# Kernel tuning notes

Measured on AMD Instinct MI355X. Metric: run time of the kernel, lower is better.

## Reference

```python
import jax, jax.numpy as jnp
import numpy as np
import math

INPUT_DIM = 1024
HIDDEN_DIM = 1024
NUM_HEADS = 16
NUM_KEYS = 4096
BATCH = 1024
BETA = 8.0


def setup_inputs() -> dict:
    key = jax.random.key(0)
    kx, kk, kv = jax.random.split(key, 3)
    bound_k = 1.0 / math.sqrt(INPUT_DIM)
    bound_v = 1.0 / math.sqrt(HIDDEN_DIM)
    x = jax.random.normal(kx, (BATCH, INPUT_DIM), dtype=jnp.float32)
    keys = jax.random.uniform(kk, (NUM_KEYS * NUM_HEADS, INPUT_DIM), dtype=jnp.float32,
                              minval=-bound_k, maxval=bound_k)
    values = jax.random.uniform(kv, (NUM_KEYS * NUM_HEADS, HIDDEN_DIM), dtype=jnp.float32,
                                minval=-bound_v, maxval=bound_v)
    return {"x": x, "keys": keys, "values": values}


def reference(x, keys, values):
    scale = math.sqrt(INPUT_DIM)
    b = x.shape[0]
    # [B, num_keys*num_heads]
    weights = (x @ keys.T) / scale
    # view as [B, num_keys, num_heads]; softmax over num_keys per head
    weights = weights.reshape(b, NUM_KEYS, NUM_HEADS)
    probs = jax.nn.softmax(BETA * weights, axis=1)
    probs = probs.reshape(b, NUM_KEYS * NUM_HEADS)
    # value retrieval
    out = probs @ values  # [B, hidden_dim]
    return out
```

## Files before the change

### kernel.cpp

```cpp
#include <hip/hip_runtime.h>
#include <hip/hip_bf16.h>
#include <stdint.h>

#define BATCH  1024
#define DIM    1024
#define NKH    65536
#define NKEYS  4096
#define HID    1024

#define SC1 0.36067376022224085f

typedef __bf16 bf16x8 __attribute__((ext_vector_type(8)));
typedef float  f32x4  __attribute__((ext_vector_type(4)));

__device__ __forceinline__ unsigned short f2bf(float f) {
  union { float f; unsigned int u; } v; v.f = f;
  unsigned int r = v.u + 0x7fffu + ((v.u >> 16) & 1u);
  return (unsigned short)(r >> 16);
}
__device__ __forceinline__ float bf2f(unsigned short s) {
  union { unsigned int u; float f; } v; v.u = ((unsigned int)s) << 16;
  return v.f;
}
__device__ __forceinline__ unsigned int pk2(float lo, float hi) {
  union { __hip_bfloat162 h; unsigned int u; } v;
  v.h = __float22bfloat162_rn(make_float2(lo, hi));
  return v.u;
}
__device__ __forceinline__ void gl2lds16(const void* g, void* l) {
  __builtin_amdgcn_global_load_lds(
      (const __attribute__((address_space(1))) void*)g,
      (__attribute__((address_space(3))) void*)l, 16, 0, 0);
}

#define KEY_GROUPS (NKH * (DIM / 8))
__global__ __launch_bounds__(256) void k_cast_all(
    const float* __restrict__ keys, const float* __restrict__ x,
    unsigned short* __restrict__ Kb, unsigned short* __restrict__ Xb) {
  int i = blockIdx.x * 256 + threadIdx.x;
  if (i < KEY_GROUPS) {
    int row = i >> 7, seg = i & 127;
    int n2 = ((row & 15) << 12) | (row >> 4);
    float4 a = ((const float4*)keys)[(size_t)i * 2];
    float4 b = ((const float4*)keys)[(size_t)i * 2 + 1];
    uint4 o;
    o.x = pk2(a.x, a.y); o.y = pk2(a.z, a.w);
    o.z = pk2(b.x, b.y); o.w = pk2(b.z, b.w);
    ((uint4*)Kb)[((size_t)n2 << 7) | seg] = o;
  } else {
    int j = i - KEY_GROUPS;
    if (j < BATCH * (DIM / 8)) {
      float4 a = ((const float4*)x)[(size_t)j * 2];
      float4 b = ((const float4*)x)[(size_t)j * 2 + 1];
      uint4 o;
      o.x = pk2(a.x, a.y); o.y = pk2(a.z, a.w);
      o.z = pk2(b.x, b.y); o.w = pk2(b.z, b.w);
      ((uint4*)Xb)[j] = o;
    }
  }
}

__global__ __launch_bounds__(256) void k_transpose_cast(
    const float* __restrict__ V, unsigned short* __restrict__ vT) {
  __shared__ float tile[64][65];
  const int t = threadIdx.x;
  const int nk0 = blockIdx.x * 64;
  const int h   = blockIdx.x >> 6;
  const int k0  = (blockIdx.x & 63) * 64;
  const int j0  = blockIdx.y * 64;
  #pragma unroll
  for (int i = 0; i < 4; ++i) {
    int idx = t + i * 256;
    int row = idx >> 4, c4 = (idx & 15) << 2;
    float4 v = *(const float4*)(V + (size_t)((k0 + row) * 16 + h) * HID + (j0 + c4));
    tile[row][c4 + 0] = v.x; tile[row][c4 + 1] = v.y;
    tile[row][c4 + 2] = v.z; tile[row][c4 + 3] = v.w;
  }
  __syncthreads();
  const int q = t & 7, jj = t >> 3;
  #pragma unroll
  for (int i = 0; i < 2; ++i) {
    int j = jj + i * 32;
    uint4 o;
    o.x = pk2(tile[q*8+0][j], tile[q*8+1][j]);
    o.y = pk2(tile[q*8+2][j], tile[q*8+3][j]);
    o.z = pk2(tile[q*8+4][j], tile[q*8+5][j]);
    o.w = pk2(tile[q*8+6][j], tile[q*8+7][j]);
    *(uint4*)(vT + (size_t)(j0 + j) * NKH + (nk0 + q*8)) = o;
  }
}

__global__ __launch_bounds__(256) void k_gemm1_exp(
    const unsigned short* __restrict__ Xb, const unsigned short* __restrict__ Kb,
    unsigned short* __restrict__ E, float* __restrict__ denom) {
  __shared__ __align__(16) unsigned short As[128 * 32];
  __shared__ __align__(16) unsigned short Bs[128 * 32];
  __shared__ float dsum[128];
  const int t = threadIdx.x;
  const int bm = blockIdx.x & 7, bn = blockIdx.x >> 3;
  const int m0 = bm << 7, n0 = bn << 7;
  const int lane = t & 63, wave = t >> 6;
  const int wm = (wave >> 1) << 6, wn = (wave & 1) << 6;
  const int r16 = lane & 15, quad = lane >> 4;
  const int srow = lane >> 2, kseg = (lane & 3) * 8;
  const int c0 = wave * 2, c1 = wave * 2 + 1;
  const unsigned short* gA0 = Xb + (size_t)(m0 + c0*16 + srow) * DIM + kseg;
  const unsigned short* gA1 = Xb + (size_t)(m0 + c1*16 + srow) * DIM + kseg;
  const unsigned short* gB0 = Kb + (size_t)(n0 + c0*16 + srow) * DIM + kseg;
  const unsigned short* gB1 = Kb + (size_t)(n0 + c1*16 + srow) * DIM + kseg;
  if (t < 128) dsum[t] = 0.0f;
  f32x4 acc[4][4] = {};
  for (int ks = 0; ks < DIM; ks += 32) {
    __syncthreads();
    gl2lds16(gA0 + ks, As + c0 * 512);
    gl2lds16(gA1 + ks, As + c1 * 512);
    gl2lds16(gB0 + ks, Bs + c0 * 512);
    gl2lds16(gB1 + ks, Bs + c1 * 512);
    __syncthreads();
    bf16x8 af[4], bfr[4];
    #pragma unroll
    for (int mi = 0; mi < 4; ++mi)
      af[mi] = *(const bf16x8*)(As + (wm + mi*16 + r16) * 32 + quad * 8);
    #pragma unroll
    for (int ni = 0; ni < 4; ++ni)
      bfr[ni] = *(const bf16x8*)(Bs + (wn + ni*16 + r16) * 32 + quad * 8);
    #pragma unroll
    for (int mi = 0; mi < 4; ++mi)
      #pragma unroll
      for (int ni = 0; ni < 4; ++ni)
        acc[mi][ni] = __builtin_amdgcn_mfma_f32_16x16x32_bf16(af[mi], bfr[ni], acc[mi][ni], 0, 0, 0);
  }
  float rs[16] = {0,0,0,0,0,0,0,0,0,0,0,0,0,0,0,0};
  #pragma unroll
  for (int mi = 0; mi < 4; ++mi) {
    #pragma unroll
    for (int ni = 0; ni < 4; ++ni) {
      #pragma unroll
      for (int v = 0; v < 4; ++v) {
        float e = exp2f(acc[mi][ni][v] * SC1);
        int row = m0 + wm + mi*16 + quad*4 + v;
        int col = n0 + wn + ni*16 + r16;
        E[(size_t)row * NKH + col] = f2bf(e);
        rs[mi*4 + v] += e;
      }
    }
  }
  #pragma unroll
  for (int m = 1; m < 16; m <<= 1)
    #pragma unroll
    for (int i = 0; i < 16; ++i) rs[i] += __shfl_xor(rs[i], m);
  if (r16 == 0) {
    #pragma unroll
    for (int i = 0; i < 16; ++i)
      atomicAdd(&dsum[wm + (i >> 2)*16 + quad*4 + (i & 3)], rs[i]);
  }
  __syncthreads();
  const int h = n0 >> 12;
  if (t < 128) atomicAdd(&denom[(size_t)(m0 + t) * 16 + h], dsum[t]);
}

__global__ __launch_bounds__(256) void k_gemm2(
    const unsigned short* __restrict__ P, const unsigned short* __restrict__ Vt,
    float* __restrict__ out, const float* __restrict__ denom) {
  __shared__ __align__(16) unsigned short As[128 * 32];
  __shared__ __align__(16) unsigned short Bs[128 * 32];
  const int t = threadIdx.x;
  const int nwg = 1024, cpx = nwg >> 3;
  const int lb = (blockIdx.x & 7) * cpx + (blockIdx.x >> 3);
  const int bm = lb & 7, bn = (lb >> 3) & 7, sp = lb >> 6;
  const int m0 = bm << 7, n0 = bn << 7;
  const size_t kb = (size_t)sp * (NKH / 16);
  const int lane = t & 63, wave = t >> 6;
  const int wm = (wave >> 1) << 6, wn = (wave & 1) << 6;
  const int r16 = lane & 15, quad = lane >> 4;
  const int srow = lane >> 2, kseg = (lane & 3) * 8;
  const int c0 = wave * 2, c1 = wave * 2 + 1;
  const unsigned short* gA0 = P  + (size_t)(m0 + c0*16 + srow) * NKH + kb + kseg;
  const unsigned short* gA1 = P  + (size_t)(m0 + c1*16 + srow) * NKH + kb + kseg;
  const unsigned short* gB0 = Vt + (size_t)(n0 + c0*16 + srow) * NKH + kb + kseg;
  const unsigned short* gB1 = Vt + (size_t)(n0 + c1*16 + srow) * NKH + kb + kseg;
  f32x4 acc[4][4] = {};
  for (int ks = 0; ks < NKH / 16; ks += 32) {
    __syncthreads();
    gl2lds16(gA0 + ks, As + c0 * 512);
    gl2lds16(gA1 + ks, As + c1 * 512);
    gl2lds16(gB0 + ks, Bs + c0 * 512);
    gl2lds16(gB1 + ks, Bs + c1 * 512);
    __syncthreads();
    bf16x8 af[4], bfr[4];
    #pragma unroll
    for (int mi = 0; mi < 4; ++mi)
      af[mi] = *(const bf16x8*)(As + (wm + mi*16 + r16) * 32 + quad * 8);
    #pragma unroll
    for (int ni = 0; ni < 4; ++ni)
      bfr[ni] = *(const bf16x8*)(Bs + (wn + ni*16 + r16) * 32 + quad * 8);
    #pragma unroll
    for (int mi = 0; mi < 4; ++mi)
      #pragma unroll
      for (int ni = 0; ni < 4; ++ni)
        acc[mi][ni] = __builtin_amdgcn_mfma_f32_16x16x32_bf16(af[mi], bfr[ni], acc[mi][ni], 0, 0, 0);
  }
  #pragma unroll
  for (int mi = 0; mi < 4; ++mi) {
    float rr[4];
    #pragma unroll
    for (int v = 0; v < 4; ++v) {
      int row = m0 + wm + mi*16 + quad*4 + v;
      rr[v] = 1.0f / denom[(size_t)row * 16 + sp];
    }
    #pragma unroll
    for (int ni = 0; ni < 4; ++ni) {
      #pragma unroll
      for (int v = 0; v < 4; ++v) {
        int row = m0 + wm + mi*16 + quad*4 + v;
        int col = n0 + wn + ni*16 + r16;
        unsafeAtomicAdd(&out[(size_t)row * HID + col], acc[mi][ni][v] * rr[v]);
      }
    }
  }
}

extern "C" void kernel_launch(void* const* d_in, const int* in_sizes, int n_in,
                              void* d_out, int out_size, void* d_ws, size_t ws_size,
                              hipStream_t stream) {
  (void)in_sizes; (void)n_in; (void)out_size; (void)ws_size;
  const float* x      = (const float*)d_in[0];
  const float* keys   = (const float*)d_in[1];
  const float* values = (const float*)d_in[2];
  float* out = (float*)d_out;

  unsigned short* E  = (unsigned short*)d_ws;
  unsigned short* B2 = E + (size_t)BATCH * NKH;
  unsigned short* Xb = B2 + (size_t)NKH * DIM;
  float* denom = (float*)(Xb + (size_t)BATCH * DIM);

  hipMemsetAsync(d_out, 0, (size_t)BATCH * HID * sizeof(float), stream);
  hipMemsetAsync(denom, 0, (size_t)BATCH * 16 * sizeof(float), stream);
  k_cast_all<<<(KEY_GROUPS + BATCH * (DIM / 8) + 255) / 256, 256, 0, stream>>>(
      keys, x, B2, Xb);
  k_gemm1_exp<<<(BATCH / 128) * (NKH / 128), 256, 0, stream>>>(Xb, B2, E, denom);
  k_transpose_cast<<<dim3(NKH / 64, HID / 64), 256, 0, stream>>>(values, B2);
  k_gemm2<<<(BATCH / 128) * (HID / 128) * 16, 256, 0, stream>>>(E, B2, out, denom);
}
```

Measured before the change: 1.037 ms.

## Rewrite both GEMMs with 256x256 tiles, double-buffered swizzled LDS pipeline

Both bf16 GEMMs now share a core with 256x256 block tiles, 512 threads, K-step 64, XOR-swizzled LDS and double buffering. Global-to-LDS loads for the next tile are interleaved with MFMA phases using partial vmcnt waits and setprio. The two memsets are folded into the cast and transpose kernels to cut launches. The larger tiles raise data reuse and overlap loads with compute, at the cost of more registers and LDS and fewer workgroups.

```diff
diff --git a/kernel.cpp b/kernel.cpp
--- a/kernel.cpp
+++ b/kernel.cpp
@@ -18,10 +18,6 @@
   unsigned int r = v.u + 0x7fffu + ((v.u >> 16) & 1u);
   return (unsigned short)(r >> 16);
 }
-__device__ __forceinline__ float bf2f(unsigned short s) {
-  union { unsigned int u; float f; } v; v.u = ((unsigned int)s) << 16;
-  return v.f;
-}
 __device__ __forceinline__ unsigned int pk2(float lo, float hi) {
   union { __hip_bfloat162 h; unsigned int u; } v;
   v.h = __float22bfloat162_rn(make_float2(lo, hi));
@@ -34,9 +30,12 @@
 }
 
 #define KEY_GROUPS (NKH * (DIM / 8))
+#define X_GROUPS   (BATCH * (DIM / 8))
+#define DN_GROUPS  (BATCH * 16 / 4)
 __global__ __launch_bounds__(256) void k_cast_all(
     const float* __restrict__ keys, const float* __restrict__ x,
-    unsigned short* __restrict__ Kb, unsigned short* __restrict__ Xb) {
+    unsigned short* __restrict__ Kb, unsigned short* __restrict__ Xb,
+    float* __restrict__ denom) {
   int i = blockIdx.x * 256 + threadIdx.x;
   if (i < KEY_GROUPS) {
     int row = i >> 7, seg = i & 127;
@@ -47,27 +46,36 @@
     o.x = pk2(a.x, a.y); o.y = pk2(a.z, a.w);
     o.z = pk2(b.x, b.y); o.w = pk2(b.z, b.w);
     ((uint4*)Kb)[((size_t)n2 << 7) | seg] = o;
+  } else if (i < KEY_GROUPS + X_GROUPS) {
+    int j = i - KEY_GROUPS;
+    float4 a = ((const float4*)x)[(size_t)j * 2];
+    float4 b = ((const float4*)x)[(size_t)j * 2 + 1];
+    uint4 o;
+    o.x = pk2(a.x, a.y); o.y = pk2(a.z, a.w);
+    o.z = pk2(b.x, b.y); o.w = pk2(b.z, b.w);
+    ((uint4*)Xb)[j] = o;
   } else {
-    int j = i - KEY_GROUPS;
-    if (j < BATCH * (DIM / 8)) {
-      float4 a = ((const float4*)x)[(size_t)j * 2];
-      float4 b = ((const float4*)x)[(size_t)j * 2 + 1];
-      uint4 o;
-      o.x = pk2(a.x, a.y); o.y = pk2(a.z, a.w);
-      o.z = pk2(b.x, b.y); o.w = pk2(b.z, b.w);
-      ((uint4*)Xb)[j] = o;
-    }
-  }
-}
-
-__global__ __launch_bounds__(256) void k_transpose_cast(
-    const float* __restrict__ V, unsigned short* __restrict__ vT) {
+    int d = i - KEY_GROUPS - X_GROUPS;
+    if (d < DN_GROUPS) ((float4*)denom)[d] = make_float4(0.f, 0.f, 0.f, 0.f);
+  }
+}
+
+__global__ __launch_bounds__(256) void k_fuse_vt(
+    const float* __restrict__ V, unsigned short* __restrict__ vT,
+    float* __restrict__ out) {
+  const int bid = blockIdx.x;
+  const int t = threadIdx.x;
+  if (bid >= 16384) {
+    int zi = (bid - 16384) * 256 + t;
+    ((float4*)out)[zi] = make_float4(0.f, 0.f, 0.f, 0.f);
+    return;
+  }
   __shared__ float tile[64][65];
-  const int t = threadIdx.x;
-  const int nk0 = blockIdx.x * 64;
-  const int h   = blockIdx.x >> 6;
-  const int k0  = (blockIdx.x & 63) * 64;
-  const int j0  = blockIdx.y * 64;
+  const int bx = bid & 1023, by = bid >> 10;
+  const int nk0 = bx * 64;
+  const int h   = bx >> 6;
+  const int k0  = (bx & 63) * 64;
+  const int j0  = by * 64;
   #pragma unroll
   for (int i = 0; i < 4; ++i) {
     int idx = t + i * 256;
@@ -90,130 +98,204 @@
   }
 }
 
-__global__ __launch_bounds__(256) void k_gemm1_exp(
+#define PH_WAIT4 do { asm volatile("s_waitcnt vmcnt(4)" ::: "memory"); \
+                      __builtin_amdgcn_s_barrier();                    \
+                      asm volatile("" ::: "memory"); } while (0)
+#define PH_BAR   do { __builtin_amdgcn_s_barrier();                    \
+                      asm volatile("" ::: "memory"); } while (0)
+
+__device__ __forceinline__ void gemm_core(
+    const unsigned short* __restrict__ A, const unsigned short* __restrict__ B,
+    size_t lda, size_t ldb, int m0, int n0, size_t k0, int nt,
+    unsigned short* As, unsigned short* Bs, f32x4 (&acc)[8][4]) {
+  const int t = threadIdx.x, lane = t & 63, w = t >> 6;
+  const int wr = w >> 2, wc = w & 3;
+  const int r16 = lane & 15, quad = lane >> 4;
+  const int srow = (w << 3) + (lane >> 3);
+  const int ksl  = (((lane & 7) ^ (lane >> 3)) << 3);
+  const int e8   = r16 & 7;
+  const int sq0  = ((quad ^ e8) << 3);
+  const int sq1  = (((4 + quad) ^ e8) << 3);
+  const unsigned short* Ag[2][2];
+  const unsigned short* Bg[2][2];
+  const int bsw = srow + (srow & 32);
+  #pragma unroll
+  for (int h = 0; h < 2; ++h)
+    #pragma unroll
+    for (int l = 0; l < 2; ++l) {
+      Ag[h][l] = A + (size_t)(m0 + h*64 + l*128 + srow) * lda + k0 + ksl;
+      Bg[h][l] = B + (size_t)(n0 + h*32 + l*128 + bsw)  * ldb + k0 + ksl;
+    }
+  const int wrow = w << 3;
+  const int boff = wrow + ((w >= 4) ? 32 : 0);
+  const int dAr[2][2] = {{ (wrow)*64,      (128 + wrow)*64 },
+                         { (64 + wrow)*64, (192 + wrow)*64 }};
+  const int dBr[2][2] = {{ (boff)*64,      (128 + boff)*64 },
+                         { (32 + boff)*64, (160 + boff)*64 }};
+  gl2lds16(Ag[0][0], As + dAr[0][0]); gl2lds16(Ag[0][1], As + dAr[0][1]);
+  gl2lds16(Bg[0][0], Bs + dBr[0][0]); gl2lds16(Bg[0][1], Bs + dBr[0][1]);
+  gl2lds16(Bg[1][0], Bs + dBr[1][0]); gl2lds16(Bg[1][1], Bs + dBr[1][1]);
+  gl2lds16(Ag[1][0], As + dAr[1][0]); gl2lds16(Ag[1][1], As + dAr[1][1]);
+
+  bf16x8 am[4][2], bn_[4][2];
+  for (int tt = 0; tt < nt; ++tt) {
+    unsigned short* Asc = As + ((tt & 1) << 14);
+    unsigned short* Bsc = Bs + ((tt & 1) << 14);
+    unsigned short* Asn = As + ((~tt & 1) << 14);
+    unsigned short* Bsn = Bs + ((~tt & 1) << 14);
+    const size_t kn = (size_t)((tt + 1 < nt) ? (tt + 1) : tt) * 64;
+    PH_WAIT4;
+    gl2lds16(Ag[0][0] + kn, Asn + dAr[0][0]);
+    gl2lds16(Ag[0][1] + kn, Asn + dAr[0][1]);
+    #pragma unroll
+    for (int mi = 0; mi < 4; ++mi) {
+      const unsigned short* p = Asc + (wr*128 + mi*16 + r16) * 64;
+      am[mi][0] = *(const bf16x8*)(p + sq0);
+      am[mi][1] = *(const bf16x8*)(p + sq1);
+    }
+    #pragma unroll
+    for (int ni = 0; ni < 2; ++ni) {
+      const unsigned short* p = Bsc + (wc*64 + ni*16 + r16) * 64;
+      bn_[ni][0] = *(const bf16x8*)(p + sq0);
+      bn_[ni][1] = *(const bf16x8*)(p + sq1);
+    }
+    __builtin_amdgcn_s_setprio(1);
+    #pragma unroll
+    for (int mi = 0; mi < 4; ++mi)
+      #pragma unroll
+      for (int ni = 0; ni < 2; ++ni) {
+        acc[mi][ni] = __builtin_amdgcn_mfma_f32_16x16x32_bf16(am[mi][0], bn_[ni][0], acc[mi][ni], 0, 0, 0);
+        acc[mi][ni] = __builtin_amdgcn_mfma_f32_16x16x32_bf16(am[mi][1], bn_[ni][1], acc[mi][ni], 0, 0, 0);
+      }
+    __builtin_amdgcn_s_setprio(0);
+    PH_WAIT4;
+    gl2lds16(Bg[0][0] + kn, Bsn + dBr[0][0]);
+    gl2lds16(Bg[0][1] + kn, Bsn + dBr[0][1]);
+    #pragma unroll
+    for (int ni = 2; ni < 4; ++ni) {
+      const unsigned short* p = Bsc + (wc*64 + ni*16 + r16) * 64;
+      bn_[ni][0] = *(const bf16x8*)(p + sq0);
+      bn_[ni][1] = *(const bf16x8*)(p + sq1);
+    }
+    __builtin_amdgcn_s_setprio(1);
+    #pragma unroll
+    for (int mi = 0; mi < 4; ++mi)
+      #pragma unroll
+      for (int ni = 2; ni < 4; ++ni) {
+        acc[mi][ni] = __builtin_amdgcn_mfma_f32_16x16x32_bf16(am[mi][0], bn_[ni][0], acc[mi][ni], 0, 0, 0);
+        acc[mi][ni] = __builtin_amdgcn_mfma_f32_16x16x32_bf16(am[mi][1], bn_[ni][1], acc[mi][ni], 0, 0, 0);
+      }
+    __builtin_amdgcn_s_setprio(0);
+    PH_WAIT4;
+    gl2lds16(Bg[1][0] + kn, Bsn + dBr[1][0]);
+    gl2lds16(Bg[1][1] + kn, Bsn + dBr[1][1]);
+    #pragma unroll
+    for (int mi = 0; mi < 4; ++mi) {
+      const unsigned short* p = Asc + (wr*128 + 64 + mi*16 + r16) * 64;
+      am[mi][0] = *(const bf16x8*)(p + sq0);
+      am[mi][1] = *(const bf16x8*)(p + sq1);
+    }
+    __builtin_amdgcn_s_setprio(1);
+    #pragma unroll
+    for (int mi = 0; mi < 4; ++mi)
+      #pragma unroll
+      for (int ni = 0; ni < 2; ++ni) {
+        acc[mi+4][ni] = __builtin_amdgcn_mfma_f32_16x16x32_bf16(am[mi][0], bn_[ni][0], acc[mi+4][ni], 0, 0, 0);
+        acc[mi+4][ni] = __builtin_amdgcn_mfma_f32_16x16x32_bf16(am[mi][1], bn_[ni][1], acc[mi+4][ni], 0, 0, 0);
+      }
+    __builtin_amdgcn_s_setprio(0);
+    PH_BAR;
+    gl2lds16(Ag[1][0] + kn, Asn + dAr[1][0]);
+    gl2lds16(Ag[1][1] + kn, Asn + dAr[1][1]);
+    __builtin_amdgcn_s_setprio(1);
+    #pragma unroll
+    for (int mi = 0; mi < 4; ++mi)
+      #pragma unroll
+      for (int ni = 2; ni < 4; ++ni) {
+        acc[mi+4][ni] = __builtin_amdgcn_mfma_f32_16x16x32_bf16(am[mi][0], bn_[ni][0], acc[mi+4][ni], 0, 0, 0);
+        acc[mi+4][ni] = __builtin_amdgcn_mfma_f32_16x16x32_bf16(am[mi][1], bn_[ni][1], acc[mi+4][ni], 0, 0, 0);
+      }
+    __builtin_amdgcn_s_setprio(0);
+  }
+}
+
+__global__ __launch_bounds__(512, 2) void k_gemm1_exp(
     const unsigned short* __restrict__ Xb, const unsigned short* __restrict__ Kb,
     unsigned short* __restrict__ E, float* __restrict__ denom) {
-  __shared__ __align__(16) unsigned short As[128 * 32];
-  __shared__ __align__(16) unsigned short Bs[128 * 32];
-  __shared__ float dsum[128];
+  __shared__ __align__(16) unsigned short As[2 * 16384];
+  __shared__ __align__(16) unsigned short Bs[2 * 16384];
+  __shared__ float dsum[256];
   const int t = threadIdx.x;
-  const int bm = blockIdx.x & 7, bn = blockIdx.x >> 3;
-  const int m0 = bm << 7, n0 = bn << 7;
-  const int lane = t & 63, wave = t >> 6;
-  const int wm = (wave >> 1) << 6, wn = (wave & 1) << 6;
+  const int bm = blockIdx.x & 3, bn = blockIdx.x >> 2;
+  const int m0 = bm << 8, n0 = bn << 8;
+  if (t < 256) dsum[t] = 0.0f;
+  f32x4 acc[8][4] = {};
+  gemm_core(Xb, Kb, DIM, DIM, m0, n0, 0, DIM / 64, As, Bs, acc);
+  const int lane = t & 63, w = t >> 6, wr = w >> 2, wc = w & 3;
   const int r16 = lane & 15, quad = lane >> 4;
-  const int srow = lane >> 2, kseg = (lane & 3) * 8;
-  const int c0 = wave * 2, c1 = wave * 2 + 1;
-  const unsigned short* gA0 = Xb + (size_t)(m0 + c0*16 + srow) * DIM + kseg;
-  const unsigned short* gA1 = Xb + (size_t)(m0 + c1*16 + srow) * DIM + kseg;
-  const unsigned short* gB0 = Kb + (size_t)(n0 + c0*16 + srow) * DIM + kseg;
-  const unsigned short* gB1 = Kb + (size_t)(n0 + c1*16 + srow) * DIM + kseg;
-  if (t < 128) dsum[t] = 0.0f;
-  f32x4 acc[4][4] = {};
-  for (int ks = 0; ks < DIM; ks += 32) {
-    __syncthreads();
-    gl2lds16(gA0 + ks, As + c0 * 512);
-    gl2lds16(gA1 + ks, As + c1 * 512);
-    gl2lds16(gB0 + ks, Bs + c0 * 512);
-    gl2lds16(gB1 + ks, Bs + c1 * 512);
-    __syncthreads();
-    bf16x8 af[4], bfr[4];
-    #pragma unroll
-    for (int mi = 0; mi < 4; ++mi)
-      af[mi] = *(const bf16x8*)(As + (wm + mi*16 + r16) * 32 + quad * 8);
-    #pragma unroll
-    for (int ni = 0; ni < 4; ++ni)
-      bfr[ni] = *(const bf16x8*)(Bs + (wn + ni*16 + r16) * 32 + quad * 8);
-    #pragma unroll
-    for (int mi = 0; mi < 4; ++mi)
-      #pragma unroll
-      for (int ni = 0; ni < 4; ++ni)
-        acc[mi][ni] = __builtin_amdgcn_mfma_f32_16x16x32_bf16(af[mi], bfr[ni], acc[mi][ni], 0, 0, 0);
-  }
-  float rs[16] = {0,0,0,0,0,0,0,0,0,0,0,0,0,0,0,0};
-  #pragma unroll
-  for (int mi = 0; mi < 4; ++mi) {
+  float rs[8][4];
+  #pragma unroll
+  for (int mi = 0; mi < 8; ++mi)
+    #pragma unroll
+    for (int v = 0; v < 4; ++v) rs[mi][v] = 0.0f;
+  #pragma unroll
+  for (int mi = 0; mi < 8; ++mi) {
     #pragma unroll
     for (int ni = 0; ni < 4; ++ni) {
       #pragma unroll
       for (int v = 0; v < 4; ++v) {
         float e = exp2f(acc[mi][ni][v] * SC1);
-        int row = m0 + wm + mi*16 + quad*4 + v;
-        int col = n0 + wn + ni*16 + r16;
+        int row = m0 + wr*128 + mi*16 + quad*4 + v;
+        int col = n0 + wc*64 + ni*16 + r16;
         E[(size_t)row * NKH + col] = f2bf(e);
-        rs[mi*4 + v] += e;
+        rs[mi][v] += e;
       }
     }
   }
   #pragma unroll
   for (int m = 1; m < 16; m <<= 1)
     #pragma unroll
-    for (int i = 0; i < 16; ++i) rs[i] += __shfl_xor(rs[i], m);
+    for (int mi = 0; mi < 8; ++mi)
+      #pragma unroll
+      for (int v = 0; v < 4; ++v) rs[mi][v] += __shfl_xor(rs[mi][v], m);
   if (r16 == 0) {
     #pragma unroll
-    for (int i = 0; i < 16; ++i)
-      atomicAdd(&dsum[wm + (i >> 2)*16 + quad*4 + (i & 3)], rs[i]);
+    for (int mi = 0; mi < 8; ++mi)
+      #pragma unroll
+      for (int v = 0; v < 4; ++v)
+        atomicAdd(&dsum[wr*128 + mi*16 + quad*4 + v], rs[mi][v]);
   }
   __syncthreads();
-  const int h = n0 >> 12;
-  if (t < 128) atomicAdd(&denom[(size_t)(m0 + t) * 16 + h], dsum[t]);
-}
-
-__global__ __launch_bounds__(256) void k_gemm2(
-    const unsigned short* __restrict__ P, const unsigned short* __restrict__ Vt,
+  if (t < 256) atomicAdd(&denom[(size_t)(m0 + t) * 16 + (bn >> 4)], dsum[t]);
+}
+
+__global__ __launch_bounds__(512, 2) void k_gemm2(
+    const unsigned short* __restrict__ E, const unsigned short* __restrict__ Vt,
     float* __restrict__ out, const float* __restrict__ denom) {
-  __shared__ __align__(16) unsigned short As[128 * 32];
-  __shared__ __align__(16) unsigned short Bs[128 * 32];
+  __shared__ __align__(16) unsigned short As[2 * 16384];
+  __shared__ __align__(16) unsigned short Bs[2 * 16384];
   const int t = threadIdx.x;
-  const int nwg = 1024, cpx = nwg >> 3;
-  const int lb = (blockIdx.x & 7) * cpx + (blockIdx.x >> 3);
-  const int bm = lb & 7, bn = (lb >> 3) & 7, sp = lb >> 6;
-  const int m0 = bm << 7, n0 = bn << 7;
-  const size_t kb = (size_t)sp * (NKH / 16);
-  const int lane = t & 63, wave = t >> 6;
-  const int wm = (wave >> 1) << 6, wn = (wave & 1) << 6;
+  const int lb = (blockIdx.x & 7) * 32 + (blockIdx.x >> 3);
+  const int bm = lb & 3, bn = (lb >> 2) & 3, sp = lb >> 4;
+  const int m0 = bm << 8, n0 = bn << 8;
+  f32x4 acc[8][4] = {};
+  gemm_core(E, Vt, NKH, NKH, m0, n0, (size_t)sp * 4096, 4096 / 64, As, Bs, acc);
+  const int lane = t & 63, w = t >> 6, wr = w >> 2, wc = w & 3;
   const int r16 = lane & 15, quad = lane >> 4;
-  const int srow = lane >> 2, kseg = (lane & 3) * 8;
-  const int c0 = wave * 2, c1 = wave * 2 + 1;
-  const unsigned short* gA0 = P  + (size_t)(m0 + c0*16 + srow) * NKH + kb + kseg;
-  const unsigned short* gA1 = P  + (size_t)(m0 + c1*16 + srow) * NKH + kb + kseg;
-  const unsigned short* gB0 = Vt + (size_t)(n0 + c0*16 + srow) * NKH + kb + kseg;
-  const unsigned short* gB1 = Vt + (size_t)(n0 + c1*16 + srow) * NKH + kb + kseg;
-  f32x4 acc[4][4] = {};
-  for (int ks = 0; ks < NKH / 16; ks += 32) {
-    __syncthreads();
-    gl2lds16(gA0 + ks, As + c0 * 512);
-    gl2lds16(gA1 + ks, As + c1 * 512);
-    gl2lds16(gB0 + ks, Bs + c0 * 512);
-    gl2lds16(gB1 + ks, Bs + c1 * 512);
-    __syncthreads();
-    bf16x8 af[4], bfr[4];
-    #pragma unroll
-    for (int mi = 0; mi < 4; ++mi)
-      af[mi] = *(const bf16x8*)(As + (wm + mi*16 + r16) * 32 + quad * 8);
-    #pragma unroll
-    for (int ni = 0; ni < 4; ++ni)
-      bfr[ni] = *(const bf16x8*)(Bs + (wn + ni*16 + r16) * 32 + quad * 8);
-    #pragma unroll
-    for (int mi = 0; mi < 4; ++mi)
-      #pragma unroll
-      for (int ni = 0; ni < 4; ++ni)
-        acc[mi][ni] = __builtin_amdgcn_mfma_f32_16x16x32_bf16(af[mi], bfr[ni], acc[mi][ni], 0, 0, 0);
-  }
-  #pragma unroll
-  for (int mi = 0; mi < 4; ++mi) {
+  #pragma unroll
+  for (int mi = 0; mi < 8; ++mi) {
     float rr[4];
     #pragma unroll
     for (int v = 0; v < 4; ++v) {
-      int row = m0 + wm + mi*16 + quad*4 + v;
+      int row = m0 + wr*128 + mi*16 + quad*4 + v;
       rr[v] = 1.0f / denom[(size_t)row * 16 + sp];
     }
     #pragma unroll
     for (int ni = 0; ni < 4; ++ni) {
       #pragma unroll
       for (int v = 0; v < 4; ++v) {
-        int row = m0 + wm + mi*16 + quad*4 + v;
-        int col = n0 + wn + ni*16 + r16;
+        int row = m0 + wr*128 + mi*16 + quad*4 + v;
+        int col = n0 + wc*64 + ni*16 + r16;
         unsafeAtomicAdd(&out[(size_t)row * HID + col], acc[mi][ni][v] * rr[v]);
       }
     }
@@ -234,11 +316,9 @@
   unsigned short* Xb = B2 + (size_t)NKH * DIM;
   float* denom = (float*)(Xb + (size_t)BATCH * DIM);
 
-  hipMemsetAsync(d_out, 0, (size_t)BATCH * HID * sizeof(float), stream);
-  hipMemsetAsync(denom, 0, (size_t)BATCH * 16 * sizeof(float), stream);
-  k_cast_all<<<(KEY_GROUPS + BATCH * (DIM / 8) + 255) / 256, 256, 0, stream>>>(
-      keys, x, B2, Xb);
-  k_gemm1_exp<<<(BATCH / 128) * (NKH / 128), 256, 0, stream>>>(Xb, B2, E, denom);
-  k_transpose_cast<<<dim3(NKH / 64, HID / 64), 256, 0, stream>>>(values, B2);
-  k_gemm2<<<(BATCH / 128) * (HID / 128) * 16, 256, 0, stream>>>(E, B2, out, denom);
-}
+  k_cast_all<<<(KEY_GROUPS + X_GROUPS + DN_GROUPS) / 256, 256, 0, stream>>>(
+      keys, x, B2, Xb, denom);
+  k_gemm1_exp<<<(BATCH / 256) * (NKH / 256), 512, 0, stream>>>(Xb, B2, E, denom);
+  k_fuse_vt<<<16384 + 1024, 256, 0, stream>>>(values, B2, out);
+  k_gemm2<<<(BATCH / 256) * (HID / 256) * 16, 512, 0, stream>>>(E, B2, out, denom);
+}
```

Result: faster. 985.4 us (-4.9%).
